# Kernel optimization log

Hardware: AMD Instinct MI355X
Metric: run time of the kernel (lower is better)

Reference implementation:

```python
import jax, jax.numpy as jnp
import numpy as np

B, T, C = 2, 2048, 2048
H, KVH = 32, 8
HD = C // H          # 64
N_REP = H // KVH     # 4


def _rotary_freq_cis(T, hd, base=10000.0):
    inv = 1.0 / (base ** (np.arange(0, hd, 2, dtype=np.float32) / hd))  # [hd/2]
    ang = np.arange(T, dtype=np.float32)[:, None] * inv[None, :]        # [T, hd/2]
    return jnp.asarray(np.stack([np.cos(ang), np.sin(ang)], axis=-1))   # [T, hd/2, 2]


def _causal_mask(T):
    m = jnp.where(jnp.tril(jnp.ones((T, T), dtype=bool)), 0.0, -1e9)
    return m[None, None].astype(jnp.float32)  # [1,1,T,T]


def setup_inputs() -> dict:
    key = jax.random.key(0)
    ks = jax.random.split(key, 5)
    s = 0.02
    return {
        "x": jax.random.normal(ks[0], (B, T, C), jnp.float32),
        "freq_cis": _rotary_freq_cis(T, HD),
        "mask": _causal_mask(T),
        "window": jnp.zeros((1, 1, T, T), jnp.float32),  # unused for Global
        "Wq": jax.random.normal(ks[1], (C, H * HD), jnp.float32) * s,
        "Wk": jax.random.normal(ks[2], (C, KVH * HD), jnp.float32) * s,
        "Wv": jax.random.normal(ks[3], (C, KVH * HD), jnp.float32) * s,
        "Wo": jax.random.normal(ks[4], (H * HD, C), jnp.float32) * s,
    }


def apply_rope(x, freq_cis):
    # x: [B, T, nH, HD]; freq_cis: [T, HD//2, 2] (cos, sin)
    xr = x.reshape(*x.shape[:-1], -1, 2)
    c = freq_cis[None, :, None, :, 0]
    s = freq_cis[None, :, None, :, 1]
    out = jnp.stack([xr[..., 0] * c - xr[..., 1] * s,
                     xr[..., 1] * c + xr[..., 0] * s], axis=-1)
    return out.reshape(x.shape).astype(x.dtype)


def reference(x, freq_cis, mask, window, Wq, Wk, Wv, Wo):
    q = (x @ Wq).reshape(B, T, H, HD)
    k = (x @ Wk).reshape(B, T, KVH, HD)
    v = (x @ Wv).reshape(B, T, KVH, HD)
    q = apply_rope(q, freq_cis)
    k = apply_rope(k, freq_cis)
    # GQA: repeat each KV head n_rep times (repeat_interleave on head dim)
    k = jnp.repeat(k, N_REP, axis=2)
    v = jnp.repeat(v, N_REP, axis=2)
    q, k, v = (t.transpose(0, 2, 1, 3) for t in (q, k, v))  # [B,H,T,HD]
    scores = jnp.einsum('bhqd,bhkd->bhqk', q, k) * (1.0 / np.sqrt(HD))
    scores = scores + mask  # Global attention type
    attn = jax.nn.softmax(scores, axis=-1)
    out = jnp.einsum('bhqk,bhkd->bhqd', attn, v)
    out = out.transpose(0, 2, 1, 3).reshape(B, T, C)
    return out @ Wo
```

## Files before the change

### kernel.cpp

```cpp
#include <hip/hip_runtime.h>


typedef short short8 __attribute__((ext_vector_type(8)));
typedef float f32x4  __attribute__((ext_vector_type(4)));

#define QSCALE 0.18033688011112042f

__device__ __forceinline__ unsigned short f2bf(float x) {
  union { float f; unsigned u; } v; v.f = x;
  unsigned r = v.u + 0x7FFFu + ((v.u >> 16) & 1u);
  return (unsigned short)(r >> 16);
}

#if __has_builtin(__builtin_amdgcn_exp2f)
#define EXP2(x) __builtin_amdgcn_exp2f(x)
#else
#define EXP2(x) exp2f(x)
#endif

__device__ __forceinline__ void gload16(const unsigned short* g, unsigned short* l) {
  __builtin_amdgcn_global_load_lds((const __attribute__((address_space(1))) void*)g,
                                   (__attribute__((address_space(3))) void*)l, 16, 0, 0);
}

__global__ __launch_bounds__(256) void cast_x_kernel(const float* __restrict__ in,
                                                     unsigned short* __restrict__ out, int n4) {
  int i = blockIdx.x * 256 + threadIdx.x;
  if (i >= n4) return;
  float4 v = ((const float4*)in)[i];
  ushort4 o; o.x = f2bf(v.x); o.y = f2bf(v.y); o.z = f2bf(v.z); o.w = f2bf(v.w);
  ((ushort4*)out)[i] = o;
}

__global__ __launch_bounds__(256) void transpose_cast(const float* __restrict__ W,
                                                      unsigned short* __restrict__ Wt,
                                                      int Ncols) {
  __shared__ float tile[32][33];
  const int nt = blockIdx.x, kt = blockIdx.y;
  const int lr = threadIdx.x >> 5, lc = threadIdx.x & 31;
  #pragma unroll
  for (int p = 0; p < 4; ++p) {
    int row = kt * 32 + lr + p * 8;
    tile[lr + p * 8][lc] = W[(size_t)row * Ncols + nt * 32 + lc];
  }
  __syncthreads();
  #pragma unroll
  for (int p = 0; p < 4; ++p) {
    int n = nt * 32 + lr + p * 8;
    Wt[(size_t)n * 2048 + kt * 32 + lc] = f2bf(tile[lc][lr + p * 8]);
  }
}

__global__ __launch_bounds__(256) void gemm128(const unsigned short* __restrict__ A,
                                               const unsigned short* __restrict__ Wt,
                                               const float* __restrict__ freq,
                                               float* __restrict__ outP,
                                               unsigned short* __restrict__ Qb,
                                               unsigned short* __restrict__ Kb,
                                               unsigned short* __restrict__ Vt,
                                               int kind) {
  __shared__ __align__(16) unsigned short As[128 * 32];
  __shared__ __align__(16) unsigned short Bs[128 * 32];
  const int tid = threadIdx.x;
  const int lane = tid & 63;
  const int wave = tid >> 6;
  const int mb = blockIdx.x, nb = blockIdx.y;
  const int m0w = (wave >> 1) * 64, n0w = (wave & 1) * 64;

  f32x4 acc[4][4];
  #pragma unroll
  for (int i = 0; i < 4; ++i)
    #pragma unroll
    for (int j = 0; j < 4; ++j)
      #pragma unroll
      for (int t = 0; t < 4; ++t) acc[i][j][t] = 0.f;

  const int ca = tid, cb = tid + 256;
  const size_t aoff0 = (size_t)(mb * 128 + (ca >> 2)) * 2048 + (ca & 3) * 8;
  const size_t aoff1 = (size_t)(mb * 128 + (cb >> 2)) * 2048 + (cb & 3) * 8;
  const size_t boff0 = (size_t)(nb * 128 + (ca >> 2)) * 2048 + (ca & 3) * 8;
  const size_t boff1 = (size_t)(nb * 128 + (cb >> 2)) * 2048 + (cb & 3) * 8;

  for (int k0 = 0; k0 < 2048; k0 += 32) {
    __syncthreads();
    gload16(A + aoff0 + k0, &As[ca * 8]);
    gload16(A + aoff1 + k0, &As[cb * 8]);
    gload16(Wt + boff0 + k0, &Bs[ca * 8]);
    gload16(Wt + boff1 + k0, &Bs[cb * 8]);
    __syncthreads();
    short8 af[4], bfr[4];
    #pragma unroll
    for (int i = 0; i < 4; ++i) {
      af[i]  = *(const short8*)&As[(m0w + i * 16 + (lane & 15)) * 32 + (lane >> 4) * 8];
      bfr[i] = *(const short8*)&Bs[(n0w + i * 16 + (lane & 15)) * 32 + (lane >> 4) * 8];
    }
    #pragma unroll
    for (int i = 0; i < 4; ++i)
      #pragma unroll
      for (int j = 0; j < 4; ++j)
        acc[i][j] = __builtin_amdgcn_mfma_f32_16x16x32_bf16(af[i], bfr[j], acc[i][j], 0, 0, 0);
  }

  const int colbase = n0w + (lane & 15);
  const int rowbase = mb * 128 + m0w + (lane >> 4) * 4;
  if (kind == 0) {
    #pragma unroll
    for (int i = 0; i < 4; ++i)
      #pragma unroll
      for (int j = 0; j < 4; ++j) {
        int col = nb * 128 + colbase + j * 16;
        #pragma unroll
        for (int t = 0; t < 4; ++t)
          outP[(size_t)(rowbase + i * 16 + t) * 2048 + col] = acc[i][j][t];
      }
  } else {
    #pragma unroll
    for (int i = 0; i < 4; ++i) {
      #pragma unroll
      for (int j = 0; j < 4; ++j) {
        int ncolg = nb * 128 + colbase + j * 16;
        f32x4 v = acc[i][j];
        if (ncolg < 2560) {
          float pv[4];
          #pragma unroll
          for (int t = 0; t < 4; ++t) pv[t] = __shfl_xor(v[t], 1);
          const int ii = (ncolg & 63) >> 1;
          const bool evn = (ncolg & 1) == 0;
          #pragma unroll
          for (int t = 0; t < 4; ++t) {
            int gm = rowbase + i * 16 + t;
            int token = gm & 2047;
            float cc = freq[(token * 32 + ii) * 2];
            float ss = freq[(token * 32 + ii) * 2 + 1];
            float o = evn ? (v[t] * cc - pv[t] * ss) : (v[t] * cc + pv[t] * ss);
            if (ncolg < 2048) Qb[(size_t)gm * 2048 + ncolg] = f2bf(o * QSCALE);
            else              Kb[(size_t)gm * 512 + (ncolg - 2048)] = f2bf(o);
          }
        } else {
          int vc = ncolg - 2560;
          int kvh = vc >> 6, d = vc & 63;
          int gm0 = rowbase + i * 16;
          int bb = gm0 >> 11, token0 = gm0 & 2047;
          ushort4 pk;
          pk.x = f2bf(v[0]); pk.y = f2bf(v[1]); pk.z = f2bf(v[2]); pk.w = f2bf(v[3]);
          *(ushort4*)&Vt[((size_t)((bb * 8 + kvh) * 64 + d)) * 2048 + token0] = pk;
        }
      }
    }
  }
}

__global__ __launch_bounds__(256) void attn_kernel(const unsigned short* __restrict__ Qb,
                                                   const unsigned short* __restrict__ Kb,
                                                   const unsigned short* __restrict__ Vt,
                                                   unsigned short* __restrict__ AO) {
  __shared__ __align__(16) char P_raw[4][4096];
  const int lane = threadIdx.x & 63;
  const int wave = threadIdx.x >> 6;
  const int blkid = blockIdx.x;
  const int kvh = blkid & 7;
  const int sl  = blkid >> 3;
  const int b   = sl >> 5;
  const int ii_ = sl & 31;
  const int qcb = ii_ & 7;
  const int h   = kvh * 4 + (ii_ >> 3);
  const int ql = lane & 15, g = lane >> 4;
  const int swz = (ql & 7) << 4;
  char* pbase = P_raw[wave];
  const unsigned short* kbase = Kb + (size_t)(b * 2048) * 512 + kvh * 64;
  const unsigned short* vbase = Vt + (size_t)((b * 8 + kvh) * 64) * 2048;

  for (int pass = 0; pass < 2; ++pass) {
    const int q0w = (pass ? (15 - qcb) : qcb) * 128 + wave * 32;
    short8 qf[2][2];
    #pragma unroll
    for (int qi = 0; qi < 2; ++qi)
      #pragma unroll
      for (int s = 0; s < 2; ++s)
        qf[qi][s] = *(const short8*)(Qb + (size_t)(b * 2048 + q0w + qi * 16 + ql) * 2048 +
                                     h * 64 + s * 32 + g * 8);
    f32x4 oacc[4][2];
    #pragma unroll
    for (int dt = 0; dt < 4; ++dt)
      #pragma unroll
      for (int qi = 0; qi < 2; ++qi)
        #pragma unroll
        for (int t = 0; t < 4; ++t) oacc[dt][qi][t] = 0.f;
    float m0 = -3e38f, m1 = -3e38f, l0 = 0.f, l1 = 0.f;

    const int nkb = (q0w >> 6) + 1;
    short8 kf[4][2], kfn[4][2];
    #pragma unroll
    for (int kt = 0; kt < 4; ++kt)
      #pragma unroll
      for (int s = 0; s < 2; ++s)
        kf[kt][s] = *(const short8*)(kbase + (size_t)(kt * 16 + ql) * 512 + s * 32 + g * 8);

    for (int kb = 0; kb < nkb; ++kb) {
      const int kv0 = kb * 64;
      f32x4 sacc[4][2];
      #pragma unroll
      for (int kt = 0; kt < 4; ++kt)
        #pragma unroll
        for (int qi = 0; qi < 2; ++qi)
          #pragma unroll
          for (int t = 0; t < 4; ++t) sacc[kt][qi][t] = 0.f;
      __builtin_amdgcn_s_setprio(1);
      #pragma unroll
      for (int kt = 0; kt < 4; ++kt)
        #pragma unroll
        for (int s = 0; s < 2; ++s)
          #pragma unroll
          for (int qi = 0; qi < 2; ++qi)
            sacc[kt][qi] = __builtin_amdgcn_mfma_f32_16x16x32_bf16(kf[kt][s], qf[qi][s],
                                                                   sacc[kt][qi], 0, 0, 0);
      __builtin_amdgcn_s_setprio(0);
      short8 vf[4][2];
      #pragma unroll
      for (int dt = 0; dt < 4; ++dt)
        #pragma unroll
        for (int c = 0; c < 2; ++c)
          vf[dt][c] = *(const short8*)(vbase + (size_t)(dt * 16 + ql) * 2048 + kv0 +
                                       c * 32 + g * 8);
      if (kb + 1 < nkb) {
        #pragma unroll
        for (int kt = 0; kt < 4; ++kt)
          #pragma unroll
          for (int s = 0; s < 2; ++s)
            kfn[kt][s] = *(const short8*)(kbase + (size_t)(kv0 + 64 + kt * 16 + ql) * 512 +
                                          s * 32 + g * 8);
      }
      if (kb == nkb - 1) {
        #pragma unroll
        for (int kt = 0; kt < 4; ++kt)
          #pragma unroll
          for (int qi = 0; qi < 2; ++qi)
            #pragma unroll
            for (int t = 0; t < 4; ++t) {
              int kv = kv0 + kt * 16 + 4 * g + t;
              if (kv > q0w + qi * 16 + ql) sacc[kt][qi][t] = -1e30f;
            }
      }
      float bm0 = sacc[0][0][0], bm1 = sacc[0][1][0];
      #pragma unroll
      for (int kt = 0; kt < 4; ++kt)
        #pragma unroll
        for (int t = 0; t < 4; ++t) {
          bm0 = fmaxf(bm0, sacc[kt][0][t]);
          bm1 = fmaxf(bm1, sacc[kt][1][t]);
        }
      bm0 = fmaxf(bm0, __shfl_xor(bm0, 16)); bm0 = fmaxf(bm0, __shfl_xor(bm0, 32));
      bm1 = fmaxf(bm1, __shfl_xor(bm1, 16)); bm1 = fmaxf(bm1, __shfl_xor(bm1, 32));
      if (!__all(bm0 <= m0 + 8.f && bm1 <= m1 + 8.f)) {
        float mn0 = fmaxf(m0, bm0), mn1 = fmaxf(m1, bm1);
        float a0 = EXP2(m0 - mn0), a1 = EXP2(m1 - mn1);
        m0 = mn0; m1 = mn1; l0 *= a0; l1 *= a1;
        #pragma unroll
        for (int dt = 0; dt < 4; ++dt)
          #pragma unroll
          for (int t = 0; t < 4; ++t) { oacc[dt][0][t] *= a0; oacc[dt][1][t] *= a1; }
      }
      float ps0 = 0.f, ps1 = 0.f;
      #pragma unroll
      for (int kt = 0; kt < 4; ++kt)
        #pragma unroll
        for (int t = 0; t < 4; ++t) {
          float e0 = EXP2(sacc[kt][0][t] - m0); sacc[kt][0][t] = e0; ps0 += e0;
          float e1 = EXP2(sacc[kt][1][t] - m1); sacc[kt][1][t] = e1; ps1 += e1;
        }
      ps0 += __shfl_xor(ps0, 16); ps0 += __shfl_xor(ps0, 32);
      ps1 += __shfl_xor(ps1, 16); ps1 += __shfl_xor(ps1, 32);
      l0 += ps0; l1 += ps1;

      #pragma unroll
      for (int qi = 0; qi < 2; ++qi)
        #pragma unroll
        for (int kt = 0; kt < 4; ++kt) {
          uint2 w;
          w.x = (unsigned)f2bf(sacc[kt][qi][0]) | ((unsigned)f2bf(sacc[kt][qi][1]) << 16);
          w.y = (unsigned)f2bf(sacc[kt][qi][2]) | ((unsigned)f2bf(sacc[kt][qi][3]) << 16);
          *(uint2*)(pbase + qi * 2048 + ((ql * 128 + kt * 32 + g * 8) ^ swz)) = w;
        }
      short8 pf[2][2];
      #pragma unroll
      for (int qi = 0; qi < 2; ++qi)
        #pragma unroll
        for (int c = 0; c < 2; ++c)
          pf[qi][c] = *(const short8*)(pbase + qi * 2048 + ((ql * 128 + c * 64 + g * 16) ^ swz));
      __builtin_amdgcn_s_setprio(1);
      #pragma unroll
      for (int dt = 0; dt < 4; ++dt)
        #pragma unroll
        for (int c = 0; c < 2; ++c)
          #pragma unroll
          for (int qi = 0; qi < 2; ++qi)
            oacc[dt][qi] = __builtin_amdgcn_mfma_f32_16x16x32_bf16(vf[dt][c], pf[qi][c],
                                                                   oacc[dt][qi], 0, 0, 0);
      __builtin_amdgcn_s_setprio(0);
      if (kb + 1 < nkb) {
        #pragma unroll
        for (int kt = 0; kt < 4; ++kt)
          #pragma unroll
          for (int s = 0; s < 2; ++s) kf[kt][s] = kfn[kt][s];
      }
    }

    const float inv0 = 1.f / l0, inv1 = 1.f / l1;
    #pragma unroll
    for (int qi = 0; qi < 2; ++qi) {
      const float inv = qi ? inv1 : inv0;
      unsigned short* ao = AO + (size_t)(b * 2048 + q0w + qi * 16 + ql) * 2048 + h * 64;
      #pragma unroll
      for (int dt = 0; dt < 4; ++dt) {
        ushort4 pk;
        pk.x = f2bf(oacc[dt][qi][0] * inv); pk.y = f2bf(oacc[dt][qi][1] * inv);
        pk.z = f2bf(oacc[dt][qi][2] * inv); pk.w = f2bf(oacc[dt][qi][3] * inv);
        *(ushort4*)&ao[dt * 16 + 4 * g] = pk;
      }
    }
  }
}

extern "C" void kernel_launch(void* const* d_in, const int* in_sizes, int n_in,
                              void* d_out, int out_size, void* d_ws, size_t ws_size,
                              hipStream_t stream) {
  const float* x    = (const float*)d_in[0];
  const float* freq = (const float*)d_in[1];
  const float* Wq = (const float*)d_in[4];
  const float* Wk = (const float*)d_in[5];
  const float* Wv = (const float*)d_in[6];
  const float* Wo = (const float*)d_in[7];
  float* out = (float*)d_out;

  char* ws = (char*)d_ws;
  unsigned short* xb   = (unsigned short*)(ws);
  unsigned short* Wqkv = (unsigned short*)(ws + 16777216);
  unsigned short* Qb   = (unsigned short*)(ws + 29360128);
  unsigned short* Kb   = (unsigned short*)(ws + 46137344);
  unsigned short* Vt   = (unsigned short*)(ws + 50331648);
  unsigned short* AO   = xb;
  unsigned short* Wot  = Wqkv;

  cast_x_kernel<<<8192, 256, 0, stream>>>(x, xb, 2097152);
  transpose_cast<<<dim3(64, 64), 256, 0, stream>>>(Wq, Wqkv, 2048);
  transpose_cast<<<dim3(16, 64), 256, 0, stream>>>(Wk, Wqkv + (size_t)2048 * 2048, 512);
  transpose_cast<<<dim3(16, 64), 256, 0, stream>>>(Wv, Wqkv + (size_t)2560 * 2048, 512);
  gemm128<<<dim3(32, 24), 256, 0, stream>>>(xb, Wqkv, freq, nullptr, Qb, Kb, Vt, 1);
  transpose_cast<<<dim3(64, 64), 256, 0, stream>>>(Wo, Wot, 2048);
  attn_kernel<<<512, 256, 0, stream>>>(Qb, Kb, Vt, AO);
  gemm128<<<dim3(32, 16), 256, 0, stream>>>(AO, Wot, freq, out, nullptr, nullptr, nullptr, 0);
}
```

Measured before the change: 431.1 us.

## Split attention into one q-chunk per block, longest first, with occupancy hint

Each attention block used to handle two paired query chunks (qcb and 15-qcb) in two passes. Now every block handles a single 128-row chunk, with twice as many blocks ordered so the longest causal chunks are dispatched first. It adds a launch-bounds hint of three blocks per CU and removes the separate kfn double buffer, reloading K into kf right after the QK MFMAs. The aim is better occupancy and tail balance, at the cost of relying on the hardware scheduler for load balance and exposing K load latency more.

New measurement: 494.9 us. 14.8% more time.

```diff
diff --git a/kernel.cpp b/kernel.cpp
--- a/kernel.cpp
+++ b/kernel.cpp
@@ -150,173 +150,165 @@
   }
 }
 
-__global__ __launch_bounds__(256) void attn_kernel(const unsigned short* __restrict__ Qb,
-                                                   const unsigned short* __restrict__ Kb,
-                                                   const unsigned short* __restrict__ Vt,
-                                                   unsigned short* __restrict__ AO) {
+__global__ __launch_bounds__(256, 3) void attn_kernel(const unsigned short* __restrict__ Qb,
+                                                      const unsigned short* __restrict__ Kb,
+                                                      const unsigned short* __restrict__ Vt,
+                                                      unsigned short* __restrict__ AO) {
   __shared__ __align__(16) char P_raw[4][4096];
   const int lane = threadIdx.x & 63;
   const int wave = threadIdx.x >> 6;
   const int blkid = blockIdx.x;
   const int kvh = blkid & 7;
-  const int sl  = blkid >> 3;
-  const int b   = sl >> 5;
-  const int ii_ = sl & 31;
-  const int qcb = ii_ & 7;
-  const int h   = kvh * 4 + (ii_ >> 3);
+  const int s   = blkid >> 3;
+  const int b   = s >> 6;
+  const int hg  = (s >> 4) & 3;
+  const int qc  = 15 - (s & 15);
+  const int h   = kvh * 4 + hg;
   const int ql = lane & 15, g = lane >> 4;
   const int swz = (ql & 7) << 4;
   char* pbase = P_raw[wave];
   const unsigned short* kbase = Kb + (size_t)(b * 2048) * 512 + kvh * 64;
   const unsigned short* vbase = Vt + (size_t)((b * 8 + kvh) * 64) * 2048;
 
-  for (int pass = 0; pass < 2; ++pass) {
-    const int q0w = (pass ? (15 - qcb) : qcb) * 128 + wave * 32;
-    short8 qf[2][2];
+  const int q0w = qc * 128 + wave * 32;
+  short8 qf[2][2];
+  #pragma unroll
+  for (int qi = 0; qi < 2; ++qi)
+    #pragma unroll
+    for (int s2 = 0; s2 < 2; ++s2)
+      qf[qi][s2] = *(const short8*)(Qb + (size_t)(b * 2048 + q0w + qi * 16 + ql) * 2048 +
+                                    h * 64 + s2 * 32 + g * 8);
+  f32x4 oacc[4][2];
+  #pragma unroll
+  for (int dt = 0; dt < 4; ++dt)
     #pragma unroll
     for (int qi = 0; qi < 2; ++qi)
       #pragma unroll
-      for (int s = 0; s < 2; ++s)
-        qf[qi][s] = *(const short8*)(Qb + (size_t)(b * 2048 + q0w + qi * 16 + ql) * 2048 +
-                                     h * 64 + s * 32 + g * 8);
-    f32x4 oacc[4][2];
+      for (int t = 0; t < 4; ++t) oacc[dt][qi][t] = 0.f;
+  float m0 = -3e38f, m1 = -3e38f, l0 = 0.f, l1 = 0.f;
+
+  const int nkb = (q0w >> 6) + 1;
+  short8 kf[4][2];
+  #pragma unroll
+  for (int kt = 0; kt < 4; ++kt)
+    #pragma unroll
+    for (int s2 = 0; s2 < 2; ++s2)
+      kf[kt][s2] = *(const short8*)(kbase + (size_t)(kt * 16 + ql) * 512 + s2 * 32 + g * 8);
+
+  for (int kb = 0; kb < nkb; ++kb) {
+    const int kv0 = kb * 64;
+    f32x4 sacc[4][2];
+    #pragma unroll
+    for (int kt = 0; kt < 4; ++kt)
+      #pragma unroll
+      for (int qi = 0; qi < 2; ++qi)
+        #pragma unroll
+        for (int t = 0; t < 4; ++t) sacc[kt][qi][t] = 0.f;
+    __builtin_amdgcn_s_setprio(1);
+    #pragma unroll
+    for (int kt = 0; kt < 4; ++kt)
+      #pragma unroll
+      for (int s2 = 0; s2 < 2; ++s2)
+        #pragma unroll
+        for (int qi = 0; qi < 2; ++qi)
+          sacc[kt][qi] = __builtin_amdgcn_mfma_f32_16x16x32_bf16(kf[kt][s2], qf[qi][s2],
+                                                                 sacc[kt][qi], 0, 0, 0);
+    __builtin_amdgcn_s_setprio(0);
+    if (kb + 1 < nkb) {
+      #pragma unroll
+      for (int kt = 0; kt < 4; ++kt)
+        #pragma unroll
+        for (int s2 = 0; s2 < 2; ++s2)
+          kf[kt][s2] = *(const short8*)(kbase + (size_t)(kv0 + 64 + kt * 16 + ql) * 512 +
+                                        s2 * 32 + g * 8);
+    }
+    short8 vf[4][2];
     #pragma unroll
     for (int dt = 0; dt < 4; ++dt)
       #pragma unroll
-      for (int qi = 0; qi < 2; ++qi)
-        #pragma unroll
-        for (int t = 0; t < 4; ++t) oacc[dt][qi][t] = 0.f;
-    float m0 = -3e38f, m1 = -3e38f, l0 = 0.f, l1 = 0.f;
-
-    const int nkb = (q0w >> 6) + 1;
-    short8 kf[4][2], kfn[4][2];
-    #pragma unroll
-    for (int kt = 0; kt < 4; ++kt)
-      #pragma unroll
-      for (int s = 0; s < 2; ++s)
-        kf[kt][s] = *(const short8*)(kbase + (size_t)(kt * 16 + ql) * 512 + s * 32 + g * 8);
-
-    for (int kb = 0; kb < nkb; ++kb) {
-      const int kv0 = kb * 64;
-      f32x4 sacc[4][2];
+      for (int c = 0; c < 2; ++c)
+        vf[dt][c] = *(const short8*)(vbase + (size_t)(dt * 16 + ql) * 2048 + kv0 +
+                                     c * 32 + g * 8);
+    if (kb == nkb - 1) {
       #pragma unroll
       for (int kt = 0; kt < 4; ++kt)
         #pragma unroll
         for (int qi = 0; qi < 2; ++qi)
           #pragma unroll
-          for (int t = 0; t < 4; ++t) sacc[kt][qi][t] = 0.f;
-      __builtin_amdgcn_s_setprio(1);
-      #pragma unroll
-      for (int kt = 0; kt < 4; ++kt)
-        #pragma unroll
-        for (int s = 0; s < 2; ++s)
-          #pragma unroll
-          for (int qi = 0; qi < 2; ++qi)
-            sacc[kt][qi] = __builtin_amdgcn_mfma_f32_16x16x32_bf16(kf[kt][s], qf[qi][s],
-                                                                   sacc[kt][qi], 0, 0, 0);
-      __builtin_amdgcn_s_setprio(0);
-      short8 vf[4][2];
+          for (int t = 0; t < 4; ++t) {
+            int kv = kv0 + kt * 16 + 4 * g + t;
+            if (kv > q0w + qi * 16 + ql) sacc[kt][qi][t] = -1e30f;
+          }
+    }
+    float bm0 = sacc[0][0][0], bm1 = sacc[0][1][0];
+    #pragma unroll
+    for (int kt = 0; kt < 4; ++kt)
+      #pragma unroll
+      for (int t = 0; t < 4; ++t) {
+        bm0 = fmaxf(bm0, sacc[kt][0][t]);
+        bm1 = fmaxf(bm1, sacc[kt][1][t]);
+      }
+    bm0 = fmaxf(bm0, __shfl_xor(bm0, 16)); bm0 = fmaxf(bm0, __shfl_xor(bm0, 32));
+    bm1 = fmaxf(bm1, __shfl_xor(bm1, 16)); bm1 = fmaxf(bm1, __shfl_xor(bm1, 32));
+    if (!__all(bm0 <= m0 + 8.f && bm1 <= m1 + 8.f)) {
+      float mn0 = fmaxf(m0, bm0), mn1 = fmaxf(m1, bm1);
+      float a0 = EXP2(m0 - mn0), a1 = EXP2(m1 - mn1);
+      m0 = mn0; m1 = mn1; l0 *= a0; l1 *= a1;
       #pragma unroll
       for (int dt = 0; dt < 4; ++dt)
         #pragma unroll
-        for (int c = 0; c < 2; ++c)
-          vf[dt][c] = *(const short8*)(vbase + (size_t)(dt * 16 + ql) * 2048 + kv0 +
-                                       c * 32 + g * 8);
-      if (kb + 1 < nkb) {
-        #pragma unroll
-        for (int kt = 0; kt < 4; ++kt)
-          #pragma unroll
-          for (int s = 0; s < 2; ++s)
-            kfn[kt][s] = *(const short8*)(kbase + (size_t)(kv0 + 64 + kt * 16 + ql) * 512 +
-                                          s * 32 + g * 8);
-      }
-      if (kb == nkb - 1) {
-        #pragma unroll
-        for (int kt = 0; kt < 4; ++kt)
-          #pragma unroll
-          for (int qi = 0; qi < 2; ++qi)
-            #pragma unroll
-            for (int t = 0; t < 4; ++t) {
-              int kv = kv0 + kt * 16 + 4 * g + t;
-              if (kv > q0w + qi * 16 + ql) sacc[kt][qi][t] = -1e30f;
-            }
-      }
-      float bm0 = sacc[0][0][0], bm1 = sacc[0][1][0];
-      #pragma unroll
-      for (int kt = 0; kt < 4; ++kt)
-        #pragma unroll
-        for (int t = 0; t < 4; ++t) {
-          bm0 = fmaxf(bm0, sacc[kt][0][t]);
-          bm1 = fmaxf(bm1, sacc[kt][1][t]);
-        }
-      bm0 = fmaxf(bm0, __shfl_xor(bm0, 16)); bm0 = fmaxf(bm0, __shfl_xor(bm0, 32));
-      bm1 = fmaxf(bm1, __shfl_xor(bm1, 16)); bm1 = fmaxf(bm1, __shfl_xor(bm1, 32));
-      if (!__all(bm0 <= m0 + 8.f && bm1 <= m1 + 8.f)) {
-        float mn0 = fmaxf(m0, bm0), mn1 = fmaxf(m1, bm1);
-        float a0 = EXP2(m0 - mn0), a1 = EXP2(m1 - mn1);
-        m0 = mn0; m1 = mn1; l0 *= a0; l1 *= a1;
-        #pragma unroll
-        for (int dt = 0; dt < 4; ++dt)
-          #pragma unroll
-          for (int t = 0; t < 4; ++t) { oacc[dt][0][t] *= a0; oacc[dt][1][t] *= a1; }
-      }
-      float ps0 = 0.f, ps1 = 0.f;
-      #pragma unroll
-      for (int kt = 0; kt < 4; ++kt)
-        #pragma unroll
-        for (int t = 0; t < 4; ++t) {
-          float e0 = EXP2(sacc[kt][0][t] - m0); sacc[kt][0][t] = e0; ps0 += e0;
-          float e1 = EXP2(sacc[kt][1][t] - m1); sacc[kt][1][t] = e1; ps1 += e1;
-        }
-      ps0 += __shfl_xor(ps0, 16); ps0 += __shfl_xor(ps0, 32);
-      ps1 += __shfl_xor(ps1, 16); ps1 += __shfl_xor(ps1, 32);
-      l0 += ps0; l1 += ps1;
-
-      #pragma unroll
-      for (int qi = 0; qi < 2; ++qi)
-        #pragma unroll
-        for (int kt = 0; kt < 4; ++kt) {
-          uint2 w;
-          w.x = (unsigned)f2bf(sacc[kt][qi][0]) | ((unsigned)f2bf(sacc[kt][qi][1]) << 16);
-          w.y = (unsigned)f2bf(sacc[kt][qi][2]) | ((unsigned)f2bf(sacc[kt][qi][3]) << 16);
-          *(uint2*)(pbase + qi * 2048 + ((ql * 128 + kt * 32 + g * 8) ^ swz)) = w;
-        }
-      short8 pf[2][2];
-      #pragma unroll
-      for (int qi = 0; qi < 2; ++qi)
-        #pragma unroll
-        for (int c = 0; c < 2; ++c)
-          pf[qi][c] = *(const short8*)(pbase + qi * 2048 + ((ql * 128 + c * 64 + g * 16) ^ swz));
-      __builtin_amdgcn_s_setprio(1);
-      #pragma unroll
-      for (int dt = 0; dt < 4; ++dt)
-        #pragma unroll
-        for (int c = 0; c < 2; ++c)
-          #pragma unroll
-          for (int qi = 0; qi < 2; ++qi)
-            oacc[dt][qi] = __builtin_amdgcn_mfma_f32_16x16x32_bf16(vf[dt][c], pf[qi][c],
-                                                                   oacc[dt][qi], 0, 0, 0);
-      __builtin_amdgcn_s_setprio(0);
-      if (kb + 1 < nkb) {
-        #pragma unroll
-        for (int kt = 0; kt < 4; ++kt)
-          #pragma unroll
-          for (int s = 0; s < 2; ++s) kf[kt][s] = kfn[kt][s];
-      }
-    }
-
-    const float inv0 = 1.f / l0, inv1 = 1.f / l1;
-    #pragma unroll
-    for (int qi = 0; qi < 2; ++qi) {
-      const float inv = qi ? inv1 : inv0;
-      unsigned short* ao = AO + (size_t)(b * 2048 + q0w + qi * 16 + ql) * 2048 + h * 64;
-      #pragma unroll
-      for (int dt = 0; dt < 4; ++dt) {
-        ushort4 pk;
-        pk.x = f2bf(oacc[dt][qi][0] * inv); pk.y = f2bf(oacc[dt][qi][1] * inv);
-        pk.z = f2bf(oacc[dt][qi][2] * inv); pk.w = f2bf(oacc[dt][qi][3] * inv);
-        *(ushort4*)&ao[dt * 16 + 4 * g] = pk;
-      }
+        for (int t = 0; t < 4; ++t) { oacc[dt][0][t] *= a0; oacc[dt][1][t] *= a1; }
+    }
+    float ps0 = 0.f, ps1 = 0.f;
+    #pragma unroll
+    for (int kt = 0; kt < 4; ++kt)
+      #pragma unroll
+      for (int t = 0; t < 4; ++t) {
+        float e0 = EXP2(sacc[kt][0][t] - m0); sacc[kt][0][t] = e0; ps0 += e0;
+        float e1 = EXP2(sacc[kt][1][t] - m1); sacc[kt][1][t] = e1; ps1 += e1;
+      }
+    ps0 += __shfl_xor(ps0, 16); ps0 += __shfl_xor(ps0, 32);
+    ps1 += __shfl_xor(ps1, 16); ps1 += __shfl_xor(ps1, 32);
+    l0 += ps0; l1 += ps1;
+
+    #pragma unroll
+    for (int qi = 0; qi < 2; ++qi)
+      #pragma unroll
+      for (int kt = 0; kt < 4; ++kt) {
+        uint2 w;
+        w.x = (unsigned)f2bf(sacc[kt][qi][0]) | ((unsigned)f2bf(sacc[kt][qi][1]) << 16);
+        w.y = (unsigned)f2bf(sacc[kt][qi][2]) | ((unsigned)f2bf(sacc[kt][qi][3]) << 16);
+        *(uint2*)(pbase + qi * 2048 + ((ql * 128 + kt * 32 + g * 8) ^ swz)) = w;
+      }
+    short8 pf[2][2];
+    #pragma unroll
+    for (int qi = 0; qi < 2; ++qi)
+      #pragma unroll
+      for (int c = 0; c < 2; ++c)
+        pf[qi][c] = *(const short8*)(pbase + qi * 2048 + ((ql * 128 + c * 64 + g * 16) ^ swz));
+    __builtin_amdgcn_s_setprio(1);
+    #pragma unroll
+    for (int dt = 0; dt < 4; ++dt)
+      #pragma unroll
+      for (int c = 0; c < 2; ++c)
+        #pragma unroll
+        for (int qi = 0; qi < 2; ++qi)
+          oacc[dt][qi] = __builtin_amdgcn_mfma_f32_16x16x32_bf16(vf[dt][c], pf[qi][c],
+                                                                 oacc[dt][qi], 0, 0, 0);
+    __builtin_amdgcn_s_setprio(0);
+  }
+
+  const float inv0 = 1.f / l0, inv1 = 1.f / l1;
+  #pragma unroll
+  for (int qi = 0; qi < 2; ++qi) {
+    const float inv = qi ? inv1 : inv0;
+    unsigned short* ao = AO + (size_t)(b * 2048 + q0w + qi * 16 + ql) * 2048 + h * 64;
+    #pragma unroll
+    for (int dt = 0; dt < 4; ++dt) {
+      ushort4 pk;
+      pk.x = f2bf(oacc[dt][qi][0] * inv); pk.y = f2bf(oacc[dt][qi][1] * inv);
+      pk.z = f2bf(oacc[dt][qi][2] * inv); pk.w = f2bf(oacc[dt][qi][3] * inv);
+      *(ushort4*)&ao[dt * 16 + 4 * g] = pk;
     }
   }
 }
@@ -347,6 +339,6 @@
   transpose_cast<<<dim3(16, 64), 256, 0, stream>>>(Wv, Wqkv + (size_t)2560 * 2048, 512);
   gemm128<<<dim3(32, 24), 256, 0, stream>>>(xb, Wqkv, freq, nullptr, Qb, Kb, Vt, 1);
   transpose_cast<<<dim3(64, 64), 256, 0, stream>>>(Wo, Wot, 2048);
-  attn_kernel<<<512, 256, 0, stream>>>(Qb, Kb, Vt, AO);
+  attn_kernel<<<1024, 256, 0, stream>>>(Qb, Kb, Vt, AO);
   gemm128<<<dim3(32, 16), 256, 0, stream>>>(AO, Wot, freq, out, nullptr, nullptr, nullptr, 0);
 }
```
